# Performance work log

Hardware: AMD Instinct MI355X
Metric: run time of the kernel (lower is better)

Reference implementation:

```python
import jax, jax.numpy as jnp
import numpy as np

EPS = 1e-5
NEG_SLOPE = 0.1


def _gcn_layer(x, row, col, W, b):
    # GCNConv, improved=True (self-loop weight 2.0), symmetric normalization.
    N = x.shape[0]
    xw = x @ W                                   # [N, H]
    ew = jnp.ones(row.shape[0], dtype=x.dtype)   # edge_weight=None -> ones
    deg = jax.ops.segment_sum(ew, col, num_segments=N) + 2.0  # +2 from improved self loop
    dinv = jax.lax.rsqrt(deg)                    # deg >= 2, always finite
    norm = dinv[row] * dinv[col]                 # [E]
    agg = jax.ops.segment_sum(norm[:, None] * xw[row], col, num_segments=N)
    agg = agg + (2.0 * dinv * dinv)[:, None] * xw  # self-loop contribution
    return agg + b


def _batchnorm(x, w, b):
    # training-mode BN over node dim (biased variance), eps=1e-5
    mu = jnp.mean(x, axis=0)
    var = jnp.mean((x - mu) ** 2, axis=0)
    return (x - mu) * jax.lax.rsqrt(var + EPS) * w + b


def setup_inputs() -> dict:
    key = jax.random.key(0)
    ks = jax.random.split(key, 10)
    N, E, F, H, OUT, G = 100000, 800000, 128, 128, 128, 2048
    x = jax.random.normal(ks[0], (N, F), dtype=jnp.float32)
    edge_index = jax.random.randint(ks[1], (2, E), 0, N, dtype=jnp.int64)
    batch = jnp.sort(jax.random.randint(ks[2], (N,), 0, G, dtype=jnp.int64))
    s1 = 1.0 / np.sqrt(F)
    s2 = 1.0 / np.sqrt(H)
    return {
        "x": x,
        "edge_index": edge_index,
        "batch": batch,
        "W1": jax.random.uniform(ks[3], (F, H), jnp.float32, -s1, s1),
        "b1": jnp.zeros((H,), jnp.float32),
        "bn1_w": jnp.ones((H,), jnp.float32),
        "bn1_b": jnp.zeros((H,), jnp.float32),
        "W2": jax.random.uniform(ks[4], (H, H), jnp.float32, -s2, s2),
        "b2": jnp.zeros((H,), jnp.float32),
        "bn2_w": jnp.ones((H,), jnp.float32),
        "bn2_b": jnp.zeros((H,), jnp.float32),
        "Wf": jax.random.uniform(ks[5], (H, OUT), jnp.float32, -s2, s2),
        "bf": jax.random.uniform(ks[6], (OUT,), jnp.float32, -s2, s2),
        "num_graphs": G,
    }


def reference(x, edge_index, batch, W1, b1, bn1_w, bn1_b, W2, b2, bn2_w, bn2_b, Wf, bf, num_graphs):
    row, col = edge_index[0], edge_index[1]
    h = _gcn_layer(x, row, col, W1, b1)
    h = jax.nn.leaky_relu(_batchnorm(h, bn1_w, bn1_b), NEG_SLOPE)
    # dropout omitted (deterministic reference / eval mode)
    h = _gcn_layer(h, row, col, W2, b2)
    h = jax.nn.leaky_relu(_batchnorm(h, bn2_w, bn2_b), NEG_SLOPE)
    pooled = jax.ops.segment_max(h, batch, num_segments=num_graphs)  # [G, H]
    pooled = jnp.where(jnp.isneginf(pooled), 0.0, pooled)            # empty graphs -> 0
    return pooled @ Wf + bf
```

## Files before the change

kernel.cpp:

```cpp
#include <hip/hip_runtime.h>
#include <hip/hip_bf16.h>

#define EPSV 1e-5f
#define SLOPE 0.1f

typedef __attribute__((ext_vector_type(8))) unsigned short ushort8v;
typedef __attribute__((ext_vector_type(8))) short bf16x8;
typedef __attribute__((ext_vector_type(4))) float f32x4;

static __device__ inline unsigned short f2bf(float f) {
    __hip_bfloat16 b = __float2bfloat16(f);
    return *reinterpret_cast<unsigned short*>(&b);
}
static __device__ inline float bf2f(unsigned short u) {
    return __uint_as_float(((unsigned)u) << 16);
}

__global__ __launch_bounds__(256) void k_count(const int* __restrict__ col,
                                               unsigned* __restrict__ cnt, int E) {
    int e = blockIdx.x * 256 + threadIdx.x;
    if (e < E) atomicAdd(&cnt[col[e]], 1u);
}

__global__ __launch_bounds__(256) void k_chunk_sum(const unsigned* __restrict__ cnt, int N,
                                                   unsigned* __restrict__ bsum,
                                                   float* __restrict__ dinv) {
    __shared__ unsigned ls[256];
    int base = blockIdx.x * 1024;
    unsigned s = 0;
    for (int i = threadIdx.x; i < 1024; i += 256) {
        int idx = base + i;
        if (idx < N) {
            unsigned c = cnt[idx];
            s += c;
            dinv[idx] = rsqrtf((float)c + 2.0f);
        }
    }
    ls[threadIdx.x] = s;
    __syncthreads();
    for (int st = 128; st > 0; st >>= 1) {
        if (threadIdx.x < st) ls[threadIdx.x] += ls[threadIdx.x + st];
        __syncthreads();
    }
    if (threadIdx.x == 0) bsum[blockIdx.x] = ls[0];
}

__global__ __launch_bounds__(128) void k_scan_bsum(unsigned* __restrict__ bsum, int nb) {
    const int t = threadIdx.x;
    unsigned v = (t < nb) ? bsum[t] : 0u;
    unsigned s = v;
    for (int d = 1; d < 64; d <<= 1) {
        unsigned y = __shfl_up(s, d, 64);
        if ((t & 63) >= d) s += y;
    }
    __shared__ unsigned wtot;
    if (t == 63) wtot = s;
    __syncthreads();
    unsigned base = (t >= 64) ? wtot : 0u;
    if (t < nb) bsum[t] = base + s - v;
}

__global__ __launch_bounds__(256) void k_scan_chunks(const unsigned* __restrict__ cnt, int N,
                                                     const unsigned* __restrict__ bsum,
                                                     int* __restrict__ off,
                                                     int* __restrict__ cursor, int E) {
    __shared__ unsigned ls[256];
    int base = blockIdx.x * 1024;
    unsigned v[4];
    unsigned s = 0;
#pragma unroll
    for (int j = 0; j < 4; j++) {
        int idx = base + threadIdx.x * 4 + j;
        v[j] = (idx < N) ? cnt[idx] : 0u;
        s += v[j];
    }
    ls[threadIdx.x] = s;
    __syncthreads();
    if (threadIdx.x == 0) {
        unsigned acc = bsum[blockIdx.x];
        for (int i = 0; i < 256; i++) { unsigned t = ls[i]; ls[i] = acc; acc += t; }
    }
    __syncthreads();
    unsigned acc = ls[threadIdx.x];
#pragma unroll
    for (int j = 0; j < 4; j++) {
        int idx = base + threadIdx.x * 4 + j;
        if (idx < N) { off[idx] = (int)acc; cursor[idx] = (int)acc; }
        acc += v[j];
    }
    if (base + threadIdx.x * 4 <= N - 1 && N - 1 < base + threadIdx.x * 4 + 4) off[N] = E;
}

__global__ __launch_bounds__(256) void k_place(const int* __restrict__ row,
                                               const int* __restrict__ col,
                                               const float* __restrict__ dinv,
                                               int* __restrict__ cursor,
                                               int2* __restrict__ spack, int E) {
    int e = blockIdx.x * 256 + threadIdx.x;
    if (e >= E) return;
    int r = row[e], c = col[e];
    int pos = atomicAdd(&cursor[c], 1);
    spack[pos] = make_int2(r, __float_as_int(dinv[r] * dinv[c]));
}

__global__ __launch_bounds__(256) void k_prepw(const float* __restrict__ W1,
                                               const float* __restrict__ W2,
                                               unsigned short* __restrict__ wT) {
    int m = blockIdx.x >> 4;
    int idx = (blockIdx.x & 15) * 256 + threadIdx.x;
    const float* W = (m == 0) ? W1 : W2;
    unsigned short* T = wT + (size_t)m * 16384;
    int k = idx >> 5, n4 = (idx & 31) * 4;
    float4 v = *(const float4*)(W + (size_t)k * 128 + n4);
    T[(size_t)(n4 + 0) * 128 + k] = f2bf(v.x);
    T[(size_t)(n4 + 1) * 128 + k] = f2bf(v.y);
    T[(size_t)(n4 + 2) * 128 + k] = f2bf(v.z);
    T[(size_t)(n4 + 3) * 128 + k] = f2bf(v.w);
}

template <int MODE>
__global__ __launch_bounds__(256) void k_gemm_m(const void* __restrict__ Xv,
                                                const unsigned short* __restrict__ wT,
                                                const float* __restrict__ sums, float invN,
                                                const float* __restrict__ bnw,
                                                const float* __restrict__ bnb,
                                                void* __restrict__ Yv, int N) {
    __shared__ unsigned short xs[64][136];
    __shared__ float sc[128], sb[128];
    const int tid = threadIdx.x;
    if (MODE == 1) {
        if (tid < 128) {
            float mu = sums[tid] * invN;
            float var = sums[128 + tid] * invN - mu * mu;
            float s = rsqrtf(var + EPSV) * bnw[tid];
            sc[tid] = s;
            sb[tid] = bnb[tid] - mu * s;
        }
        __syncthreads();
    }
    const int base = blockIdx.x * 64;
    if (MODE == 1) {
        const unsigned short* Xh = (const unsigned short*)Xv;
        for (int i = tid; i < 1024; i += 256) {
            int r = i >> 4, c8 = (i & 15) * 8;
            int row = base + r; if (row >= N) row = N - 1;
            ushort8v v = *(const ushort8v*)(Xh + (size_t)row * 128 + c8);
            ushort8v o;
#pragma unroll
            for (int j = 0; j < 8; j++) {
                float f = fmaf(bf2f(v[j]), sc[c8 + j], sb[c8 + j]);
                f = f > 0.f ? f : SLOPE * f;
                o[j] = f2bf(f);
            }
            *(ushort8v*)(&xs[r][c8]) = o;
        }
    } else {
        const float* X = (const float*)Xv;
        for (int i = tid; i < 2048; i += 256) {
            int r = i >> 5, c4 = i & 31;
            int row = base + r; if (row >= N) row = N - 1;
            float4 v = ((const float4*)(X + (size_t)row * 128))[c4];
            ushort4 o;
            o.x = f2bf(v.x); o.y = f2bf(v.y); o.z = f2bf(v.z); o.w = f2bf(v.w);
            *(ushort4*)(&xs[r][c4 * 4]) = o;
        }
    }
    __syncthreads();

    const int lane = tid & 63;
    const int m0 = (tid >> 6) * 16;
    const int mr = lane & 15;
    const int kg = lane >> 4;
    f32x4 acc[8];
#pragma unroll
    for (int nf = 0; nf < 8; nf++) acc[nf] = (f32x4){0.f, 0.f, 0.f, 0.f};

#pragma unroll
    for (int kt = 0; kt < 4; kt++) {
        bf16x8 a = *(const bf16x8*)(&xs[m0 + mr][kt * 32 + kg * 8]);
#pragma unroll
        for (int nf = 0; nf < 8; nf++) {
            bf16x8 b = *(const bf16x8*)(wT + (size_t)(nf * 16 + mr) * 128 + kt * 32 + kg * 8);
            acc[nf] = __builtin_amdgcn_mfma_f32_16x16x32_bf16(a, b, acc[nf], 0, 0, 0);
        }
    }

    __syncthreads();
#pragma unroll
    for (int nf = 0; nf < 8; nf++) {
#pragma unroll
        for (int r = 0; r < 4; r++) {
            xs[m0 + kg * 4 + r][nf * 16 + mr] = f2bf(acc[nf][r]);
        }
    }
    __syncthreads();
    unsigned short* Yh = (unsigned short*)Yv;
    for (int i = tid; i < 1024; i += 256) {
        int r = i >> 4, c8 = (i & 15) * 8;
        int row = base + r;
        if (row < N)
            *(ushort8v*)(Yh + (size_t)row * 128 + c8) = *(const ushort8v*)(&xs[r][c8]);
    }
}

__global__ __launch_bounds__(256) void k_agg5(const unsigned short* __restrict__ xwh,
                                              const int* __restrict__ off,
                                              const int2* __restrict__ spack,
                                              const float* __restrict__ dinv,
                                              const float* __restrict__ bias,
                                              unsigned short* __restrict__ h,
                                              float* __restrict__ sums, int N) {
    __shared__ float ls1[128], ls2[128];
    const int tid = threadIdx.x;
    if (tid < 128) { ls1[tid] = 0.f; ls2[tid] = 0.f; }
    __syncthreads();

    const int q = tid & 15;
    const int grp = (blockIdx.x * 256 + tid) >> 4;
    const int nGrp = gridDim.x * 16;

    float bj[8];
#pragma unroll
    for (int j = 0; j < 8; j++) bj[j] = bias[q * 8 + j];
    float st1[8] = {0, 0, 0, 0, 0, 0, 0, 0};
    float st2[8] = {0, 0, 0, 0, 0, 0, 0, 0};

    for (int n = grp; n < N; n += nGrp) {
        const int s = off[n], e = off[n + 1];
        float a[8] = {0, 0, 0, 0, 0, 0, 0, 0};
        int i = s;
        for (; i + 8 <= e; i += 8) {
            int2 p0 = spack[i + 0], p1 = spack[i + 1], p2 = spack[i + 2], p3 = spack[i + 3];
            int2 p4 = spack[i + 4], p5 = spack[i + 5], p6 = spack[i + 6], p7 = spack[i + 7];
            ushort8v v0 = *(const ushort8v*)(xwh + (size_t)p0.x * 128 + q * 8);
            ushort8v v1 = *(const ushort8v*)(xwh + (size_t)p1.x * 128 + q * 8);
            ushort8v v2 = *(const ushort8v*)(xwh + (size_t)p2.x * 128 + q * 8);
            ushort8v v3 = *(const ushort8v*)(xwh + (size_t)p3.x * 128 + q * 8);
            ushort8v v4 = *(const ushort8v*)(xwh + (size_t)p4.x * 128 + q * 8);
            ushort8v v5 = *(const ushort8v*)(xwh + (size_t)p5.x * 128 + q * 8);
            ushort8v v6 = *(const ushort8v*)(xwh + (size_t)p6.x * 128 + q * 8);
            ushort8v v7 = *(const ushort8v*)(xwh + (size_t)p7.x * 128 + q * 8);
            float n0 = __int_as_float(p0.y), n1 = __int_as_float(p1.y);
            float n2 = __int_as_float(p2.y), n3 = __int_as_float(p3.y);
            float n4 = __int_as_float(p4.y), n5 = __int_as_float(p5.y);
            float n6 = __int_as_float(p6.y), n7 = __int_as_float(p7.y);
#pragma unroll
            for (int j = 0; j < 8; j++) {
                float t = fmaf(n0, bf2f(v0[j]), fmaf(n1, bf2f(v1[j]),
                          fmaf(n2, bf2f(v2[j]), n3 * bf2f(v3[j]))));
                float u = fmaf(n4, bf2f(v4[j]), fmaf(n5, bf2f(v5[j]),
                          fmaf(n6, bf2f(v6[j]), n7 * bf2f(v7[j]))));
                a[j] += t + u;
            }
        }
        for (; i + 4 <= e; i += 4) {
            int2 p0 = spack[i + 0], p1 = spack[i + 1], p2 = spack[i + 2], p3 = spack[i + 3];
            ushort8v v0 = *(const ushort8v*)(xwh + (size_t)p0.x * 128 + q * 8);
            ushort8v v1 = *(const ushort8v*)(xwh + (size_t)p1.x * 128 + q * 8);
            ushort8v v2 = *(const ushort8v*)(xwh + (size_t)p2.x * 128 + q * 8);
            ushort8v v3 = *(const ushort8v*)(xwh + (size_t)p3.x * 128 + q * 8);
            float n0 = __int_as_float(p0.y), n1 = __int_as_float(p1.y);
            float n2 = __int_as_float(p2.y), n3 = __int_as_float(p3.y);
#pragma unroll
            for (int j = 0; j < 8; j++) {
                a[j] += fmaf(n0, bf2f(v0[j]), fmaf(n1, bf2f(v1[j]),
                        fmaf(n2, bf2f(v2[j]), n3 * bf2f(v3[j]))));
            }
        }
        for (; i < e; ++i) {
            int2 p = spack[i];
            ushort8v v = *(const ushort8v*)(xwh + (size_t)p.x * 128 + q * 8);
            float nm = __int_as_float(p.y);
#pragma unroll
            for (int j = 0; j < 8; j++) a[j] = fmaf(nm, bf2f(v[j]), a[j]);
        }
        float dc = dinv[n];
        float sl = 2.f * dc * dc;
        ushort8v xv = *(const ushort8v*)(xwh + (size_t)n * 128 + q * 8);
        ushort8v ov;
#pragma unroll
        for (int j = 0; j < 8; j++) {
            float o = fmaf(sl, bf2f(xv[j]), a[j]) + bj[j];
            st1[j] += o;
            st2[j] += o * o;
            ov[j] = f2bf(o);
        }
        *(ushort8v*)(h + (size_t)n * 128 + q * 8) = ov;
    }
#pragma unroll
    for (int j = 0; j < 8; j++) {
        atomicAdd(&ls1[q * 8 + j], st1[j]);
        atomicAdd(&ls2[q * 8 + j], st2[j]);
    }
    __syncthreads();
    if (tid < 128) {
        atomicAdd(&sums[tid], ls1[tid]);
        atomicAdd(&sums[128 + tid], ls2[tid]);
    }
}

__global__ __launch_bounds__(256) void k_tail(const unsigned short* __restrict__ h,
                                              const int* __restrict__ batch,
                                              const float* __restrict__ sums, float invN,
                                              const float* __restrict__ bnw,
                                              const float* __restrict__ bnb,
                                              const float* __restrict__ Wf,
                                              const float* __restrict__ bf,
                                              float* __restrict__ out, int N, int G) {
    const int lane = threadIdx.x & 63;
    const int g = blockIdx.x * 4 + (threadIdx.x >> 6);
    if (g >= G) return;
    const int f0 = lane, f1 = lane + 64;
    float mu0 = sums[f0] * invN;
    float var0 = sums[128 + f0] * invN - mu0 * mu0;
    float sc0 = rsqrtf(var0 + EPSV) * bnw[f0];
    float sb0 = bnb[f0] - mu0 * sc0;
    float mu1 = sums[f1] * invN;
    float var1 = sums[128 + f1] * invN - mu1 * mu1;
    float sc1 = rsqrtf(var1 + EPSV) * bnw[f1];
    float sb1 = bnb[f1] - mu1 * sc1;

    int lo, hi;
    { int a = 0, b = N; while (a < b) { int m = (a + b) >> 1; if (batch[m] < g) a = m + 1; else b = m; } lo = a; }
    { int a = lo, b = N; while (a < b) { int m = (a + b) >> 1; if (batch[m] < g + 1) a = m + 1; else b = m; } hi = a; }

    float m0 = -__builtin_inff(), m1 = -__builtin_inff();
    for (int n = lo; n < hi; n++) {
        float v0 = fmaf(bf2f(h[(size_t)n * 128 + f0]), sc0, sb0);
        float v1 = fmaf(bf2f(h[(size_t)n * 128 + f1]), sc1, sb1);
        v0 = v0 > 0.f ? v0 : SLOPE * v0;
        v1 = v1 > 0.f ? v1 : SLOPE * v1;
        m0 = fmaxf(m0, v0);
        m1 = fmaxf(m1, v1);
    }
    if (lo >= hi) { m0 = 0.f; m1 = 0.f; }

    float o0 = bf[f0], o1 = bf[f1];
    for (int k = 0; k < 64; k++) {
        float vk = __shfl(m0, k, 64);
        o0 = fmaf(vk, Wf[(size_t)k * 128 + f0], o0);
        o1 = fmaf(vk, Wf[(size_t)k * 128 + f1], o1);
    }
    for (int k = 0; k < 64; k++) {
        float vk = __shfl(m1, k, 64);
        o0 = fmaf(vk, Wf[(size_t)(k + 64) * 128 + f0], o0);
        o1 = fmaf(vk, Wf[(size_t)(k + 64) * 128 + f1], o1);
    }
    out[(size_t)g * 128 + f0] = o0;
    out[(size_t)g * 128 + f1] = o1;
}

extern "C" void kernel_launch(void* const* d_in, const int* in_sizes, int n_in,
                              void* d_out, int out_size, void* d_ws, size_t ws_size,
                              hipStream_t stream) {
    const float* x     = (const float*)d_in[0];
    const int*   ei    = (const int*)d_in[1];
    const int*   batch = (const int*)d_in[2];
    const float* W1    = (const float*)d_in[3];
    const float* b1    = (const float*)d_in[4];
    const float* bn1w  = (const float*)d_in[5];
    const float* bn1b  = (const float*)d_in[6];
    const float* W2    = (const float*)d_in[7];
    const float* b2    = (const float*)d_in[8];
    const float* bn2w  = (const float*)d_in[9];
    const float* bn2b  = (const float*)d_in[10];
    const float* Wf    = (const float*)d_in[11];
    const float* bf    = (const float*)d_in[12];

    const int N = in_sizes[0] / 128;
    const int E = in_sizes[1] / 2;
    const int G = out_size / 128;
    const int* rowp = ei;
    const int* colp = ei + E;
    float* out = (float*)d_out;
    const float invN = 1.0f / N;

    char* w = (char*)d_ws;
    unsigned short* bufAh = (unsigned short*)w; w += (size_t)N * 128 * 2;
    unsigned short* bufBh = (unsigned short*)w; w += (size_t)N * 128 * 2;
    float*    dinv   = (float*)w;    w += (size_t)N * 4;
    unsigned* cnt    = (unsigned*)w; w += (size_t)N * 4;
    int*      cursor = (int*)w;      w += (size_t)N * 4;
    int*      off    = (int*)w;      w += (size_t)(N + 4) * 4;
    unsigned* bsum   = (unsigned*)w; w += 1024 * 4;
    int2*     spack  = (int2*)w;     w += (size_t)E * 8;
    float*    sums   = (float*)w;    w += 512 * 4;
    unsigned short* wT = (unsigned short*)w; w += 2 * 16384 * 2;

    float* sums1 = sums;
    float* sums2 = sums + 256;
    const int nb = (N + 1023) / 1024;

    hipMemsetAsync(cnt, 0, (size_t)N * 4, stream);
    hipMemsetAsync(sums, 0, 512 * 4, stream);
    k_prepw<<<32, 256, 0, stream>>>(W1, W2, wT);
    k_count<<<(E + 255) / 256, 256, 0, stream>>>(colp, cnt, E);
    k_chunk_sum<<<nb, 256, 0, stream>>>(cnt, N, bsum, dinv);
    k_scan_bsum<<<1, 128, 0, stream>>>(bsum, nb);
    k_scan_chunks<<<nb, 256, 0, stream>>>(cnt, N, bsum, off, cursor, E);
    k_place<<<(E + 255) / 256, 256, 0, stream>>>(rowp, colp, dinv, cursor, spack, E);

    const int aggBlocks = 2048;
    const int gemmGrid = (N + 63) / 64;

    k_gemm_m<0><<<gemmGrid, 256, 0, stream>>>(x, wT, nullptr, 0.f, nullptr, nullptr,
                                              bufAh, N);
    k_agg5<<<aggBlocks, 256, 0, stream>>>(bufAh, off, spack, dinv, b1, bufBh, sums1, N);

    k_gemm_m<1><<<gemmGrid, 256, 0, stream>>>(bufBh, wT + 16384, sums1, invN, bn1w, bn1b,
                                              bufAh, N);
    k_agg5<<<aggBlocks, 256, 0, stream>>>(bufAh, off, spack, dinv, b2, bufBh, sums2, N);

    k_tail<<<(G + 3) / 4, 256, 0, stream>>>(bufBh, batch, sums2, invN, bn2w, bn2b,
                                            Wf, bf, out, N, G);
}
```

Baseline: 426.0 us.

## Sort destination nodes by in-degree to balance aggregation work across wavefronts

Adds a degree histogram, scan and placement pass that builds a permutation of nodes grouped by in-degree. Each entry packs node id, CSR offsets and dinv. The aggregation kernel walks nodes in this order, so the 16-lane groups in a wavefront handle nodes of similar degree and diverge less on loop trip counts. The cost is three extra small kernels and an extra 16-byte load per node. Output rows are also written in scattered order, so locality of the self-row reads and writes may suffer.

```diff
diff --git a/kernel.cpp b/kernel.cpp
--- a/kernel.cpp
+++ b/kernel.cpp
@@ -101,6 +101,49 @@
     int r = row[e], c = col[e];
     int pos = atomicAdd(&cursor[c], 1);
     spack[pos] = make_int2(r, __float_as_int(dinv[r] * dinv[c]));
+}
+
+__global__ __launch_bounds__(256) void k_hist(const unsigned* __restrict__ cnt, int N,
+                                              unsigned* __restrict__ hist) {
+    __shared__ unsigned lh[256];
+    lh[threadIdx.x] = 0;
+    __syncthreads();
+    int n = blockIdx.x * 256 + threadIdx.x;
+    if (n < N) {
+        unsigned d = cnt[n]; if (d > 255u) d = 255u;
+        atomicAdd(&lh[d], 1u);
+    }
+    __syncthreads();
+    if (lh[threadIdx.x]) atomicAdd(&hist[threadIdx.x], lh[threadIdx.x]);
+}
+
+__global__ __launch_bounds__(256) void k_permscan(const unsigned* __restrict__ hist,
+                                                  int* __restrict__ binCur) {
+    const int t = threadIdx.x;
+    unsigned v = hist[t];
+    unsigned s = v;
+    for (int d = 1; d < 64; d <<= 1) {
+        unsigned y = __shfl_up(s, d, 64);
+        if ((t & 63) >= d) s += y;
+    }
+    __shared__ unsigned wtot[4];
+    if ((t & 63) == 63) wtot[t >> 6] = s;
+    __syncthreads();
+    unsigned carry = 0;
+    for (int w = 0; w < (t >> 6); w++) carry += wtot[w];
+    binCur[t] = (int)(carry + s - v);
+}
+
+__global__ __launch_bounds__(256) void k_permplace(const unsigned* __restrict__ cnt,
+                                                   const int* __restrict__ off,
+                                                   const float* __restrict__ dinv,
+                                                   int* __restrict__ binCur,
+                                                   int4* __restrict__ perm4, int N) {
+    int n = blockIdx.x * 256 + threadIdx.x;
+    if (n >= N) return;
+    unsigned d = cnt[n]; if (d > 255u) d = 255u;
+    int pos = atomicAdd(&binCur[d], 1);
+    perm4[pos] = make_int4(n, off[n], off[n + 1], __float_as_int(dinv[n]));
 }
 
 __global__ __launch_bounds__(256) void k_prepw(const float* __restrict__ W1,
@@ -204,9 +247,8 @@
 }
 
 __global__ __launch_bounds__(256) void k_agg5(const unsigned short* __restrict__ xwh,
-                                              const int* __restrict__ off,
+                                              const int4* __restrict__ perm4,
                                               const int2* __restrict__ spack,
-                                              const float* __restrict__ dinv,
                                               const float* __restrict__ bias,
                                               unsigned short* __restrict__ h,
                                               float* __restrict__ sums, int N) {
@@ -225,8 +267,10 @@
     float st1[8] = {0, 0, 0, 0, 0, 0, 0, 0};
     float st2[8] = {0, 0, 0, 0, 0, 0, 0, 0};
 
-    for (int n = grp; n < N; n += nGrp) {
-        const int s = off[n], e = off[n + 1];
+    for (int idx = grp; idx < N; idx += nGrp) {
+        int4 pm = perm4[idx];
+        const int n = pm.x, s = pm.y, e = pm.z;
+        const float dc = __int_as_float(pm.w);
         float a[8] = {0, 0, 0, 0, 0, 0, 0, 0};
         int i = s;
         for (; i + 8 <= e; i += 8) {
@@ -274,7 +318,6 @@
 #pragma unroll
             for (int j = 0; j < 8; j++) a[j] = fmaf(nm, bf2f(v[j]), a[j]);
         }
-        float dc = dinv[n];
         float sl = 2.f * dc * dc;
         ushort8v xv = *(const ushort8v*)(xwh + (size_t)n * 128 + q * 8);
         ushort8v ov;
@@ -385,31 +428,38 @@
     unsigned* bsum   = (unsigned*)w; w += 1024 * 4;
     int2*     spack  = (int2*)w;     w += (size_t)E * 8;
     float*    sums   = (float*)w;    w += 512 * 4;
+    unsigned* hist   = (unsigned*)w; w += 256 * 4;
+    int*      binCur = (int*)w;      w += 256 * 4;
+    int4*     perm4  = (int4*)w;     w += (size_t)N * 16;
     unsigned short* wT = (unsigned short*)w; w += 2 * 16384 * 2;
 
     float* sums1 = sums;
     float* sums2 = sums + 256;
     const int nb = (N + 1023) / 1024;
+    const int nblk = (N + 255) / 256;
 
     hipMemsetAsync(cnt, 0, (size_t)N * 4, stream);
-    hipMemsetAsync(sums, 0, 512 * 4, stream);
+    hipMemsetAsync(sums, 0, (512 + 256) * 4, stream);
     k_prepw<<<32, 256, 0, stream>>>(W1, W2, wT);
     k_count<<<(E + 255) / 256, 256, 0, stream>>>(colp, cnt, E);
     k_chunk_sum<<<nb, 256, 0, stream>>>(cnt, N, bsum, dinv);
     k_scan_bsum<<<1, 128, 0, stream>>>(bsum, nb);
     k_scan_chunks<<<nb, 256, 0, stream>>>(cnt, N, bsum, off, cursor, E);
     k_place<<<(E + 255) / 256, 256, 0, stream>>>(rowp, colp, dinv, cursor, spack, E);
+    k_hist<<<nblk, 256, 0, stream>>>(cnt, N, hist);
+    k_permscan<<<1, 256, 0, stream>>>(hist, binCur);
+    k_permplace<<<nblk, 256, 0, stream>>>(cnt, off, dinv, binCur, perm4, N);
 
     const int aggBlocks = 2048;
     const int gemmGrid = (N + 63) / 64;
 
     k_gemm_m<0><<<gemmGrid, 256, 0, stream>>>(x, wT, nullptr, 0.f, nullptr, nullptr,
                                               bufAh, N);
-    k_agg5<<<aggBlocks, 256, 0, stream>>>(bufAh, off, spack, dinv, b1, bufBh, sums1, N);
+    k_agg5<<<aggBlocks, 256, 0, stream>>>(bufAh, perm4, spack, b1, bufBh, sums1, N);
 
     k_gemm_m<1><<<gemmGrid, 256, 0, stream>>>(bufBh, wT + 16384, sums1, invN, bn1w, bn1b,
                                               bufAh, N);
-    k_agg5<<<aggBlocks, 256, 0, stream>>>(bufAh, off, spack, dinv, b2, bufBh, sums2, N);
+    k_agg5<<<aggBlocks, 256, 0, stream>>>(bufAh, perm4, spack, b2, bufBh, sums2, N);
 
     k_tail<<<(G + 3) / 4, 256, 0, stream>>>(bufBh, batch, sums2, invN, bn2w, bn2b,
                                             Wf, bf, out, N, G);
```

New measurement: 771.7 us. 81.1% more time.
